# Optimization experiments

Measured on AMD Instinct MI355X. Metric: run time of the kernel, lower is better.

The kernel has to match this reference:

```python
import jax, jax.numpy as jnp
import numpy as np

D_MODEL, KAN_HIDDEN, NUM, K = 1024, 128, 3, 3  # grid_size=3, spline order k=3
GRID_RANGE = (-1.0, 1.0)


def make_grid(in_dim):
    # extended grid: num+1 interior knots padded by k steps of h on each side -> num+1+2k points
    h = (GRID_RANGE[1] - GRID_RANGE[0]) / NUM
    g = jnp.arange(-K, NUM + K + 1, dtype=jnp.float32) * h + GRID_RANGE[0]  # [num+1+2k]
    return jnp.broadcast_to(g, (in_dim, g.shape[0]))  # [in_dim, G]


def b_splines(x, grid):
    # Cox-de-Boor recursion. x: [N, D], grid: [D, G] -> basis [N, D, G-1-K]
    xg = x[:, :, None]  # [N, D, 1]
    B = ((xg >= grid[None, :, :-1]) & (xg < grid[None, :, 1:])).astype(x.dtype)
    for d in range(1, K + 1):
        left = (xg - grid[None, :, : -(d + 1)]) / (grid[:, d:-1] - grid[:, : -(d + 1)])[None]
        right = (grid[None, :, d + 1:] - xg) / (grid[:, d + 1:] - grid[:, 1:-d])[None]
        B = left * B[:, :, :-1] + right * B[:, :, 1:]
    return B  # [N, D, NUM+K]


def kan_layer(x, grid, coef, scale_base, scale_sp):
    # y[n,i,o] = scale_base[i,o]*silu(x[n,i]) + scale_sp[i,o]*sum_g B[n,i,g]*coef[i,o,g]; out = y.sum(i)
    B = b_splines(x, grid)  # [N, in, NUM+K]
    spline = jnp.einsum('nig,iog->no', B, coef * scale_sp[:, :, None])
    base = jnp.einsum('ni,io->no', jax.nn.silu(x), scale_base)
    return base + spline  # [N, out]


def setup_inputs() -> dict:
    key = jax.random.key(0)
    ks = jax.random.split(key, 7)
    s = 0.1  # small init scale for spline coefficients, matching noisy init spirit
    return {
        'x': jax.random.normal(ks[0], (4, 4096, D_MODEL), dtype=jnp.float32),
        'coef1': jax.random.normal(ks[1], (D_MODEL, KAN_HIDDEN, NUM + K), dtype=jnp.float32) * s,
        'scale_base1': jax.random.normal(ks[2], (D_MODEL, KAN_HIDDEN), dtype=jnp.float32),
        'scale_sp1': jnp.ones((D_MODEL, KAN_HIDDEN), dtype=jnp.float32),
        'coef2': jax.random.normal(ks[3], (KAN_HIDDEN, D_MODEL, NUM + K), dtype=jnp.float32) * s,
        'scale_base2': jax.random.normal(ks[4], (KAN_HIDDEN, D_MODEL), dtype=jnp.float32),
        'scale_sp2': jnp.ones((KAN_HIDDEN, D_MODEL), dtype=jnp.float32),
    }


def reference(x, coef1, scale_base1, scale_sp1, coef2, scale_base2, scale_sp2):
    b, s, d = x.shape
    xf = x.reshape(-1, d)  # [N, d_model]
    g1 = make_grid(D_MODEL)
    g2 = make_grid(KAN_HIDDEN)
    y1 = kan_layer(xf, g1, coef1, scale_base1, scale_sp1)   # [N, kan_hidden]
    y2 = kan_layer(y1, g2, coef2, scale_base2, scale_sp2)   # [N, d_model]
    return y2.reshape(b, s, d)
```

## Files before the change

kernel.cpp:

```cpp
#include <hip/hip_runtime.h>
#include <stdint.h>

typedef float f32x4 __attribute__((ext_vector_type(4)));
typedef __bf16 bf16x8 __attribute__((ext_vector_type(8)));

#define NROW 16384
#define DM   1024
#define HID  128
#define K1   8192
#define K2   1024

__device__ __forceinline__ unsigned short f2bf(float f) {
  unsigned u = __builtin_bit_cast(unsigned, f);
  u += 0x7fffu + ((u >> 16) & 1u);
  return (unsigned short)(u >> 16);
}

__device__ __forceinline__ uint32_t pkbf(float lo, float hi) {
  return (uint32_t)f2bf(lo) | ((uint32_t)f2bf(hi) << 16);
}

__device__ __forceinline__ void g2l16(const void* g, void* l) {
  __builtin_amdgcn_global_load_lds(
      (const __attribute__((address_space(1))) unsigned int*)g,
      (__attribute__((address_space(3))) unsigned int*)l, 16, 0, 0);
}

__device__ __forceinline__ bf16x8 expand8(float v) {
  const float t = (v + 3.0f) * 1.5f;
  const float cf = floorf(t);
  const float u = t - cf;
  int c = (int)cf;
  c = c < -1 ? -1 : c;
  c = c > 9 ? 9 : c;
  const float u2 = u * u, u3 = u2 * u, omu = 1.0f - u;
  const float p0 = u3 * (1.0f / 6.0f);
  const float p1 = (1.0f / 6.0f) + 0.5f * u + 0.5f * u2 - 0.5f * u3;
  const float p2 = (4.0f / 6.0f) - u2 + 0.5f * u3;
  const float p3 = omu * omu * omu * (1.0f / 6.0f);
  const uint64_t W = (uint64_t)pkbf(p3, p2) | ((uint64_t)pkbf(p1, p0) << 32);
  const int sa = (c - 2) * 16;
  const int sl = sa & 63;
  const uint64_t t1 = W << sl;
  const uint64_t t2 = (W >> (63 - sl)) >> 1;
  const uint64_t t3 = W >> ((-sa) & 63);
  const uint64_t L = sa < 0 ? t3 : (sa < 64 ? t1 : 0);
  const uint64_t H = sa < 0 ? 0  : (sa < 64 ? t2 : t1);
  const float s = v * __frcp_rn(1.0f + __expf(-v));
  const unsigned short sh = f2bf(s);
  const float shf = __builtin_bit_cast(float, (uint32_t)sh << 16);
  const unsigned short slo = f2bf(s - shf);
  const uint32_t w0 = ((uint32_t)L & 0xffff0000u) | sh;
  const uint32_t w1 = (uint32_t)(L >> 32);
  const uint32_t w2 = (uint32_t)H;
  const uint32_t w3 = ((uint32_t)(H >> 32) & 0xffffu) | ((uint32_t)slo << 16);
  union { uint4 q; bf16x8 b; } r;
  r.q = (uint4){w0, w1, w2, w3};
  return r.b;
}

__global__ void kan_prep_w1(const float* __restrict__ c1, const float* __restrict__ sb1,
                            const float* __restrict__ sp1, unsigned short* __restrict__ w1t) {
  const int t = blockIdx.x * 256 + threadIdx.x;
  const int o = t >> 10, i = t & 1023;
  const float sb = sb1[i * HID + o], sp = sp1[i * HID + o];
  const float* cf = c1 + (size_t)(i * HID + o) * 6;
  union { uint4 u; unsigned short h[8]; } r;
  const unsigned short b = f2bf(sb);
  r.h[0] = b; r.h[7] = b;
#pragma unroll
  for (int g = 0; g < 6; ++g) r.h[g + 1] = f2bf(cf[g] * sp);
  *(uint4*)(w1t + (size_t)o * K1 + i * 8) = r.u;
}

__global__ void kan_prep_w2(const float* __restrict__ c2, const float* __restrict__ sb2,
                            const float* __restrict__ sp2, unsigned short* __restrict__ w2t) {
  const int t = blockIdx.x * 256 + threadIdx.x;
  const int o = t >> 7, i = t & 127;
  const float sb = sb2[i * DM + o], sp = sp2[i * DM + o];
  const float* cf = c2 + (size_t)(i * DM + o) * 6;
  union { uint4 u; unsigned short h[8]; } r;
  const unsigned short b = f2bf(sb);
  r.h[0] = b; r.h[7] = b;
#pragma unroll
  for (int g = 0; g < 6; ++g) r.h[g + 1] = f2bf(cf[g] * sp);
  *(uint4*)(w2t + (size_t)o * K2 + i * 8) = r.u;
}

__global__ __launch_bounds__(512, 2) void kan_gemm1(
    const float* __restrict__ x, const unsigned short* __restrict__ w1t,
    float* __restrict__ yp) {
  __shared__ __align__(16) char lds[65536];
  const int tid = threadIdx.x;
  const int lane = tid & 63, w = tid >> 6;
  const int wk = w >> 2, wm = (w >> 1) & 1, wn = w & 1;
  const int mt = blockIdx.x >> 1, kh = blockIdx.x & 1;
  const int m0 = mt * 128;
  const int arow = tid >> 2, acs = (tid & 3) * 2;

  f32x4 acc[4][4];
#pragma unroll
  for (int a = 0; a < 4; ++a)
#pragma unroll
    for (int b = 0; b < 4; ++b) acc[a][b] = (f32x4){0.f, 0.f, 0.f, 0.f};

  const int bo = wn * 64 + (lane & 15);
  const int bk = wk * 32 + (lane >> 4) * 8;

  auto loadB = [&](int kt, bf16x8* bfrag) {
#pragma unroll
    for (int ni = 0; ni < 4; ++ni)
      bfrag[ni] = *(const bf16x8*)(w1t + (size_t)(bo + ni * 16) * K1 + kh * 4096 + kt * 64 + bk);
  };
  auto stageA = [&](float2 xv, int buf) {
    bf16x8 u0 = expand8(xv.x);
    bf16x8 u1 = expand8(xv.y);
    char* base = lds + buf * 16384;
    const int sw = (arow & 7) << 4;
    *(bf16x8*)(base + ((arow * 128 + acs * 16) ^ sw)) = u0;
    *(bf16x8*)(base + ((arow * 128 + acs * 16 + 16) ^ sw)) = u1;
  };

  const float* xrow = x + (size_t)(m0 + arow) * DM + kh * 512 + acs;
  bf16x8 bcur[4], bnxt[4];
  float2 xv = *(const float2*)xrow;
  loadB(0, bcur);
  stageA(xv, 0);
  xv = *(const float2*)(xrow + 8);
  __syncthreads();

  const int NT = 64;
  for (int kt = 0; kt < NT; ++kt) {
    const int cur = kt & 1;
    if (kt + 1 < NT) {
      loadB(kt + 1, bnxt);
      stageA(xv, cur ^ 1);
      if (kt + 2 < NT) xv = *(const float2*)(xrow + (kt + 2) * 8);
    }
    const char* ab = lds + cur * 16384;
    bf16x8 af[4];
#pragma unroll
    for (int mi = 0; mi < 4; ++mi) {
      const int row = wm * 64 + mi * 16 + (lane & 15);
      af[mi] = *(const bf16x8*)(ab + ((row * 128 + wk * 64 + (lane >> 4) * 16) ^ ((row & 7) << 4)));
    }
#pragma unroll
    for (int mi = 0; mi < 4; ++mi)
#pragma unroll
      for (int ni = 0; ni < 4; ++ni)
        acc[mi][ni] = __builtin_amdgcn_mfma_f32_16x16x32_bf16(af[mi], bcur[ni], acc[mi][ni], 0, 0, 0);
    __syncthreads();
#pragma unroll
    for (int ni = 0; ni < 4; ++ni) bcur[ni] = bnxt[ni];
  }

  if (wk == 1) {
    char* r = lds + (w & 3) * 16384;
#pragma unroll
    for (int mi = 0; mi < 4; ++mi)
#pragma unroll
      for (int ni = 0; ni < 4; ++ni)
        *(f32x4*)(r + (mi * 4 + ni) * 1024 + lane * 16) = acc[mi][ni];
  }
  __syncthreads();
  if (wk == 0) {
    const char* r = lds + w * 16384;
    float* yb = yp + (size_t)kh * NROW * HID;
#pragma unroll
    for (int mi = 0; mi < 4; ++mi)
#pragma unroll
      for (int ni = 0; ni < 4; ++ni) {
        f32x4 o = *(const f32x4*)(r + (mi * 4 + ni) * 1024 + lane * 16);
        o += acc[mi][ni];
        const int col = wn * 64 + ni * 16 + (lane & 15);
#pragma unroll
        for (int rr = 0; rr < 4; ++rr) {
          const int row = wm * 64 + mi * 16 + (lane >> 4) * 4 + rr;
          yb[(size_t)(m0 + row) * HID + col] = o[rr];
        }
      }
  }
}

__global__ void kan_combine(const float* __restrict__ yp, unsigned short* __restrict__ a2) {
  const size_t i = (size_t)blockIdx.x * 256 + threadIdx.x;
  const float v = yp[i] + yp[i + (size_t)NROW * HID];
  bf16x8 u = expand8(v);
  *(bf16x8*)(a2 + i * 8) = u;
}

__global__ __launch_bounds__(256, 2) void kan_gemm2(
    const unsigned short* __restrict__ a2, const unsigned short* __restrict__ w2t,
    float* __restrict__ out) {
  __shared__ __align__(16) unsigned short lds[2 * 16384];
  const int tid = threadIdx.x;
  const int lane = tid & 63, w = tid >> 6;
  const int wm = w >> 1, wn = w & 1;
  const int mt = blockIdx.x & 127, nt = blockIdx.x >> 7;
  const int m0 = mt * 128, n0 = nt * 128;

  f32x4 acc[4][4];
#pragma unroll
  for (int a = 0; a < 4; ++a)
#pragma unroll
    for (int b = 0; b < 4; ++b) acc[a][b] = (f32x4){0.f, 0.f, 0.f, 0.f};

  auto stage = [&](int kt, int buf) {
#pragma unroll
    for (int q = 0; q < 4; ++q) {
      const int r = (w * 4 + q) * 8 + (lane >> 3);
      const int slot = (lane & 7) ^ (lane >> 3);
      g2l16(a2 + (size_t)(m0 + r) * K2 + kt * 64 + slot * 8,
            (char*)lds + buf * 32768 + (w * 4 + q) * 1024);
      g2l16(w2t + (size_t)(n0 + r) * K2 + kt * 64 + slot * 8,
            (char*)lds + buf * 32768 + 16384 + (w * 4 + q) * 1024);
    }
  };

  stage(0, 0);
  __syncthreads();
  for (int kt = 0; kt < 16; ++kt) {
    const int cur = kt & 1;
    if (kt + 1 < 16) stage(kt + 1, cur ^ 1);
    const char* ab = (const char*)lds + cur * 32768;
    const char* bb = ab + 16384;
#pragma unroll
    for (int ks = 0; ks < 2; ++ks) {
      bf16x8 af[4], bfr[4];
#pragma unroll
      for (int mi = 0; mi < 4; ++mi) {
        const int row = wm * 64 + mi * 16 + (lane & 15);
        af[mi] = *(const bf16x8*)(ab + ((row * 128 + ks * 64 + (lane >> 4) * 16) ^ ((row & 7) << 4)));
      }
#pragma unroll
      for (int ni = 0; ni < 4; ++ni) {
        const int col = wn * 64 + ni * 16 + (lane & 15);
        bfr[ni] = *(const bf16x8*)(bb + ((col * 128 + ks * 64 + (lane >> 4) * 16) ^ ((col & 7) << 4)));
      }
#pragma unroll
      for (int mi = 0; mi < 4; ++mi)
#pragma unroll
        for (int ni = 0; ni < 4; ++ni)
          acc[mi][ni] = __builtin_amdgcn_mfma_f32_16x16x32_bf16(af[mi], bfr[ni], acc[mi][ni], 0, 0, 0);
    }
    __syncthreads();
  }

#pragma unroll
  for (int mi = 0; mi < 4; ++mi)
#pragma unroll
    for (int r = 0; r < 4; ++r) {
      const int row = wm * 64 + mi * 16 + (lane >> 4) * 4 + r;
#pragma unroll
      for (int ni = 0; ni < 4; ++ni) {
        const int col = wn * 64 + ni * 16 + (lane & 15);
        out[(size_t)(m0 + row) * DM + n0 + col] = acc[mi][ni][r];
      }
    }
}

extern "C" void kernel_launch(void* const* d_in, const int* in_sizes, int n_in,
                              void* d_out, int out_size, void* d_ws, size_t ws_size,
                              hipStream_t stream) {
  const float* x   = (const float*)d_in[0];
  const float* c1  = (const float*)d_in[1];
  const float* sb1 = (const float*)d_in[2];
  const float* sp1 = (const float*)d_in[3];
  const float* c2  = (const float*)d_in[4];
  const float* sb2 = (const float*)d_in[5];
  const float* sp2 = (const float*)d_in[6];
  float* out = (float*)d_out;

  unsigned short* w1t = (unsigned short*)d_ws;
  unsigned short* w2t = w1t + (size_t)HID * K1;
  unsigned short* a2  = w2t + (size_t)DM * K2;
  float*          yp  = (float*)(a2 + (size_t)NROW * K2);

  kan_prep_w1<<<512, 256, 0, stream>>>(c1, sb1, sp1, w1t);
  kan_prep_w2<<<512, 256, 0, stream>>>(c2, sb2, sp2, w2t);
  kan_gemm1<<<256, 512, 0, stream>>>(x, w1t, yp);
  kan_combine<<<NROW * HID / 256, 256, 0, stream>>>(yp, a2);
  kan_gemm2<<<(NROW / 128) * (DM / 128), 256, 0, stream>>>(a2, w2t, out);
}
```

Before: 130.5 us.

## Halve GEMM1 M-tile, unroll double-buffer, use native bf16 cvt, relax GEMM2 waits

GEMM1 now uses 64-row tiles, launching 512 blocks instead of 256, with half the LDS and a launch bound of 4 blocks per CU to raise occupancy. Its main loop is manually unrolled by two with ping-pong B registers, and each thread expands one x value per step instead of two. The bf16 packing switches to native __bf16 conversions so the hardware cvt instruction can be used. GEMM2 replaces __syncthreads with explicit vmcnt waits and raw s_barrier so async global-to-LDS loads for the next stage can stay in flight across the barrier. The trade-off is that each B tile is reused across fewer rows in GEMM1, so more B loads are issued per output.

```diff
diff --git a/kernel.cpp b/kernel.cpp
--- a/kernel.cpp
+++ b/kernel.cpp
@@ -3,6 +3,7 @@
 
 typedef float f32x4 __attribute__((ext_vector_type(4)));
 typedef __bf16 bf16x8 __attribute__((ext_vector_type(8)));
+typedef __bf16 bf16x2 __attribute__((ext_vector_type(2)));
 
 #define NROW 16384
 #define DM   1024
@@ -16,8 +17,11 @@
   return (unsigned short)(u >> 16);
 }
 
-__device__ __forceinline__ uint32_t pkbf(float lo, float hi) {
-  return (uint32_t)f2bf(lo) | ((uint32_t)f2bf(hi) << 16);
+__device__ __forceinline__ uint32_t pk2(float lo, float hi) {
+  bf16x2 v;
+  v[0] = (__bf16)lo;
+  v[1] = (__bf16)hi;
+  return __builtin_bit_cast(uint32_t, v);
 }
 
 __device__ __forceinline__ void g2l16(const void* g, void* l) {
@@ -38,7 +42,7 @@
   const float p1 = (1.0f / 6.0f) + 0.5f * u + 0.5f * u2 - 0.5f * u3;
   const float p2 = (4.0f / 6.0f) - u2 + 0.5f * u3;
   const float p3 = omu * omu * omu * (1.0f / 6.0f);
-  const uint64_t W = (uint64_t)pkbf(p3, p2) | ((uint64_t)pkbf(p1, p0) << 32);
+  const uint64_t W = (uint64_t)pk2(p3, p2) | ((uint64_t)pk2(p1, p0) << 32);
   const int sa = (c - 2) * 16;
   const int sl = sa & 63;
   const uint64_t t1 = W << sl;
@@ -47,13 +51,13 @@
   const uint64_t L = sa < 0 ? t3 : (sa < 64 ? t1 : 0);
   const uint64_t H = sa < 0 ? 0  : (sa < 64 ? t2 : t1);
   const float s = v * __frcp_rn(1.0f + __expf(-v));
-  const unsigned short sh = f2bf(s);
-  const float shf = __builtin_bit_cast(float, (uint32_t)sh << 16);
-  const unsigned short slo = f2bf(s - shf);
+  const uint32_t sh = (uint32_t)__builtin_bit_cast(unsigned short, (__bf16)s);
+  const float shf = __builtin_bit_cast(float, sh << 16);
+  const uint32_t slo = (uint32_t)__builtin_bit_cast(unsigned short, (__bf16)(s - shf));
   const uint32_t w0 = ((uint32_t)L & 0xffff0000u) | sh;
   const uint32_t w1 = (uint32_t)(L >> 32);
   const uint32_t w2 = (uint32_t)H;
-  const uint32_t w3 = ((uint32_t)(H >> 32) & 0xffffu) | ((uint32_t)slo << 16);
+  const uint32_t w3 = ((uint32_t)(H >> 32) & 0xffffu) | (slo << 16);
   union { uint4 q; bf16x8 b; } r;
   r.q = (uint4){w0, w1, w2, w3};
   return r.b;
@@ -87,87 +91,87 @@
   *(uint4*)(w2t + (size_t)o * K2 + i * 8) = r.u;
 }
 
-__global__ __launch_bounds__(512, 2) void kan_gemm1(
+__global__ __launch_bounds__(512, 4) void kan_gemm1(
     const float* __restrict__ x, const unsigned short* __restrict__ w1t,
     float* __restrict__ yp) {
-  __shared__ __align__(16) char lds[65536];
+  __shared__ __align__(16) char lds[32768];
   const int tid = threadIdx.x;
   const int lane = tid & 63, w = tid >> 6;
   const int wk = w >> 2, wm = (w >> 1) & 1, wn = w & 1;
   const int mt = blockIdx.x >> 1, kh = blockIdx.x & 1;
-  const int m0 = mt * 128;
-  const int arow = tid >> 2, acs = (tid & 3) * 2;
-
-  f32x4 acc[4][4];
-#pragma unroll
-  for (int a = 0; a < 4; ++a)
+  const int m0 = mt * 64;
+  const int arow = tid >> 3, acol = tid & 7;
+
+  f32x4 acc[2][4];
+#pragma unroll
+  for (int a = 0; a < 2; ++a)
 #pragma unroll
     for (int b = 0; b < 4; ++b) acc[a][b] = (f32x4){0.f, 0.f, 0.f, 0.f};
 
   const int bo = wn * 64 + (lane & 15);
-  const int bk = wk * 32 + (lane >> 4) * 8;
-
-  auto loadB = [&](int kt, bf16x8* bfrag) {
-#pragma unroll
-    for (int ni = 0; ni < 4; ++ni)
-      bfrag[ni] = *(const bf16x8*)(w1t + (size_t)(bo + ni * 16) * K1 + kh * 4096 + kt * 64 + bk);
-  };
-  auto stageA = [&](float2 xv, int buf) {
-    bf16x8 u0 = expand8(xv.x);
-    bf16x8 u1 = expand8(xv.y);
-    char* base = lds + buf * 16384;
-    const int sw = (arow & 7) << 4;
-    *(bf16x8*)(base + ((arow * 128 + acs * 16) ^ sw)) = u0;
-    *(bf16x8*)(base + ((arow * 128 + acs * 16 + 16) ^ sw)) = u1;
-  };
-
-  const float* xrow = x + (size_t)(m0 + arow) * DM + kh * 512 + acs;
-  bf16x8 bcur[4], bnxt[4];
-  float2 xv = *(const float2*)xrow;
-  loadB(0, bcur);
-  stageA(xv, 0);
-  xv = *(const float2*)(xrow + 8);
+  const unsigned short* bp = w1t + (size_t)bo * K1 + kh * 4096 + wk * 32 + (lane >> 4) * 8;
+
+  char* wa0 = lds + ((arow * 128 + acol * 16) ^ ((arow & 7) << 4));
+  char* wa1 = wa0 + 8192;
+  const char* ra0[2];
+#pragma unroll
+  for (int mi = 0; mi < 2; ++mi) {
+    const int row = wm * 32 + mi * 16 + (lane & 15);
+    ra0[mi] = lds + ((row * 128 + wk * 64 + (lane >> 4) * 16) ^ ((row & 7) << 4));
+  }
+  const float* xp = x + (size_t)(m0 + arow) * DM + kh * 512 + acol;
+
+  bf16x8 b0[4], b1[4], af[2];
+  float xv;
+
+#define LOADB(dst, kt)                                                        \
+  _Pragma("unroll") for (int ni = 0; ni < 4; ++ni)                            \
+      dst[ni] = *(const bf16x8*)(bp + (size_t)ni * 16 * K1 + (kt) * 64);
+
+#define MFMA_TILE(bb, roff)                                                   \
+  _Pragma("unroll") for (int mi = 0; mi < 2; ++mi)                            \
+      af[mi] = *(const bf16x8*)(ra0[mi] + roff);                              \
+  _Pragma("unroll") for (int mi = 0; mi < 2; ++mi)                            \
+  _Pragma("unroll") for (int ni = 0; ni < 4; ++ni)                            \
+      acc[mi][ni] = __builtin_amdgcn_mfma_f32_16x16x32_bf16(af[mi], bb[ni],   \
+                                                            acc[mi][ni], 0, 0, 0);
+
+  LOADB(b0, 0);
+  *(bf16x8*)wa0 = expand8(xp[0]);
+  xv = xp[8];
   __syncthreads();
 
-  const int NT = 64;
-  for (int kt = 0; kt < NT; ++kt) {
-    const int cur = kt & 1;
-    if (kt + 1 < NT) {
-      loadB(kt + 1, bnxt);
-      stageA(xv, cur ^ 1);
-      if (kt + 2 < NT) xv = *(const float2*)(xrow + (kt + 2) * 8);
-    }
-    const char* ab = lds + cur * 16384;
-    bf16x8 af[4];
-#pragma unroll
-    for (int mi = 0; mi < 4; ++mi) {
-      const int row = wm * 64 + mi * 16 + (lane & 15);
-      af[mi] = *(const bf16x8*)(ab + ((row * 128 + wk * 64 + (lane >> 4) * 16) ^ ((row & 7) << 4)));
-    }
-#pragma unroll
-    for (int mi = 0; mi < 4; ++mi)
-#pragma unroll
-      for (int ni = 0; ni < 4; ++ni)
-        acc[mi][ni] = __builtin_amdgcn_mfma_f32_16x16x32_bf16(af[mi], bcur[ni], acc[mi][ni], 0, 0, 0);
+  for (int kt = 0; kt < 64; kt += 2) {
+    LOADB(b1, kt + 1);
+    *(bf16x8*)wa1 = expand8(xv);
+    xv = xp[(kt + 2 < 64 ? kt + 2 : 63) * 8];
+    MFMA_TILE(b0, 0)
     __syncthreads();
-#pragma unroll
-    for (int ni = 0; ni < 4; ++ni) bcur[ni] = bnxt[ni];
-  }
+    if (kt + 2 < 64) {
+      LOADB(b0, kt + 2);
+      *(bf16x8*)wa0 = expand8(xv);
+      xv = xp[(kt + 3 < 64 ? kt + 3 : 63) * 8];
+    }
+    MFMA_TILE(b1, 8192)
+    __syncthreads();
+  }
+#undef LOADB
+#undef MFMA_TILE
 
   if (wk == 1) {
-    char* r = lds + (w & 3) * 16384;
-#pragma unroll
-    for (int mi = 0; mi < 4; ++mi)
+    char* r = lds + (w & 3) * 8192;
+#pragma unroll
+    for (int mi = 0; mi < 2; ++mi)
 #pragma unroll
       for (int ni = 0; ni < 4; ++ni)
         *(f32x4*)(r + (mi * 4 + ni) * 1024 + lane * 16) = acc[mi][ni];
   }
   __syncthreads();
   if (wk == 0) {
-    const char* r = lds + w * 16384;
+    const char* r = lds + w * 8192;
     float* yb = yp + (size_t)kh * NROW * HID;
 #pragma unroll
-    for (int mi = 0; mi < 4; ++mi)
+    for (int mi = 0; mi < 2; ++mi)
 #pragma unroll
       for (int ni = 0; ni < 4; ++ni) {
         f32x4 o = *(const f32x4*)(r + (mi * 4 + ni) * 1024 + lane * 16);
@@ -175,7 +179,7 @@
         const int col = wn * 64 + ni * 16 + (lane & 15);
 #pragma unroll
         for (int rr = 0; rr < 4; ++rr) {
-          const int row = wm * 64 + mi * 16 + (lane >> 4) * 4 + rr;
+          const int row = wm * 32 + mi * 16 + (lane >> 4) * 4 + rr;
           yb[(size_t)(m0 + row) * HID + col] = o[rr];
         }
       }
@@ -218,10 +222,16 @@
   };
 
   stage(0, 0);
-  __syncthreads();
   for (int kt = 0; kt < 16; ++kt) {
     const int cur = kt & 1;
-    if (kt + 1 < 16) stage(kt + 1, cur ^ 1);
+    if (kt + 1 < 16) {
+      stage(kt + 1, cur ^ 1);
+      asm volatile("s_waitcnt vmcnt(8)" ::: "memory");
+    } else {
+      asm volatile("s_waitcnt vmcnt(0)" ::: "memory");
+    }
+    __builtin_amdgcn_sched_barrier(0);
+    __builtin_amdgcn_s_barrier();
     const char* ab = (const char*)lds + cur * 32768;
     const char* bb = ab + 16384;
 #pragma unroll
@@ -243,7 +253,7 @@
         for (int ni = 0; ni < 4; ++ni)
           acc[mi][ni] = __builtin_amdgcn_mfma_f32_16x16x32_bf16(af[mi], bfr[ni], acc[mi][ni], 0, 0, 0);
     }
-    __syncthreads();
+    __builtin_amdgcn_s_barrier();
   }
 
 #pragma unroll
@@ -278,7 +288,7 @@
 
   kan_prep_w1<<<512, 256, 0, stream>>>(c1, sb1, sp1, w1t);
   kan_prep_w2<<<512, 256, 0, stream>>>(c2, sb2, sp2, w2t);
-  kan_gemm1<<<256, 512, 0, stream>>>(x, w1t, yp);
+  kan_gemm1<<<512, 512, 0, stream>>>(x, w1t, yp);
   kan_combine<<<NROW * HID / 256, 256, 0, stream>>>(yp, a2);
   kan_gemm2<<<(NROW / 128) * (DM / 128), 256, 0, stream>>>(a2, w2t, out);
 }
```

After: 180.2 us. 1.38x slower.
